# Performance work log

Measured on AMD Instinct MI355X. Metric: run time of the kernel, lower is better.

## Reference

```python
import jax, jax.numpy as jnp
import numpy as np

EMBED_DIM = 1024
NUM_HEADS = 16
HEAD_DIM = EMBED_DIM // NUM_HEADS


def setup_inputs() -> dict:
    key = jax.random.key(0)
    ks = jax.random.split(key, 5)
    B, S, D = 2, 2048, EMBED_DIM
    bound_qkv = 1.0 / np.sqrt(D)
    bound_out = 1.0 / np.sqrt(D)
    return {
        "x": jax.random.normal(ks[0], (B, S, D), dtype=jnp.float32),
        "w_qkv": jax.random.uniform(ks[1], (3 * D, D), jnp.float32, -bound_qkv, bound_qkv),
        "b_qkv": jax.random.uniform(ks[2], (3 * D,), jnp.float32, -bound_qkv, bound_qkv),
        "w_out": jax.random.uniform(ks[3], (D, D), jnp.float32, -bound_out, bound_out),
        "b_out": jax.random.uniform(ks[4], (D,), jnp.float32, -bound_out, bound_out),
    }


def reference(x, w_qkv, b_qkv, w_out, b_out):
    B, S, D = x.shape
    H, Hd = NUM_HEADS, HEAD_DIM
    qkv = x @ w_qkv.T + b_qkv                      # [B,S,3D]
    q, k, v = jnp.split(qkv, 3, axis=-1)           # each [B,S,D]
    # [B,S,D] -> [B,H,S,Hd]
    q = q.reshape(B, S, H, Hd).transpose(0, 2, 1, 3)
    k = k.reshape(B, S, H, Hd).transpose(0, 2, 1, 3)
    v = v.reshape(B, S, H, Hd).transpose(0, 2, 1, 3)
    scores = jnp.einsum("bhqd,bhkd->bhqk", q, k) / np.sqrt(Hd).astype(np.float32)
    probs = jax.nn.softmax(scores, axis=-1)
    attn = jnp.einsum("bhqk,bhkd->bhqd", probs, v)  # [B,H,S,Hd]
    attn = attn.transpose(0, 2, 1, 3).reshape(B, S, D)
    return attn @ w_out.T + b_out
```

## Files before the change

### kernel.cpp

```cpp
#include <hip/hip_runtime.h>

typedef __bf16 bf16_t;
typedef bf16_t bf16x4 __attribute__((ext_vector_type(4)));
typedef bf16_t bf16x8 __attribute__((ext_vector_type(8)));
typedef float f32x4 __attribute__((ext_vector_type(4)));
typedef float f32x16 __attribute__((ext_vector_type(16)));
typedef unsigned short u16;

#define MFMA16(a, b, c) __builtin_amdgcn_mfma_f32_16x16x32_bf16((a), (b), (c), 0, 0, 0)
#define MFMA32(a, b, c) __builtin_amdgcn_mfma_f32_32x32x16_bf16((a), (b), (c), 0, 0, 0)

#define BATCH 2
#define SEQ   2048
#define DIM   1024
#define NH    16
#define HD    64
#define ROWS  (BATCH * SEQ)
#define QKVN  (3 * DIM)
#define GK    1024

__device__ __forceinline__ u16 f2bf(float f) {
    unsigned u = __float_as_uint(f);
    u += 0x7FFFu + ((u >> 16) & 1u);
    return (u16)(u >> 16);
}

__device__ __forceinline__ float exp2_fast(float x) {
    float r;
    asm("v_exp_f32 %0, %1" : "=v"(r) : "v"(x));
    return r;
}

#define PKBF(lo_, hi_) ({ unsigned r_; \
    asm("v_cvt_pk_bf16_f32 %0, %1, %2" : "=v"(r_) : "v"(lo_), "v"(hi_)); r_; })
#define PLSWAP(a_, b_) \
    asm volatile("v_permlane32_swap_b32 %0, %1" : "+v"(a_), "+v"(b_))

#define GLDS(src, dst) __builtin_amdgcn_global_load_lds( \
    (const __attribute__((address_space(1))) void*)(src), \
    (__attribute__((address_space(3))) void*)(dst), 16, 0, 0)

#define WAITB(n) do { \
    asm volatile("s_waitcnt vmcnt(" #n ")" ::: "memory"); \
    __builtin_amdgcn_s_barrier(); } while (0)

__global__ __launch_bounds__(256) void cvt_kernel(
    const float* __restrict__ x,  u16* __restrict__ xb,  int nx4,
    const float* __restrict__ w1, u16* __restrict__ w1b, int n14,
    const float* __restrict__ w2, u16* __restrict__ w2b, int n24)
{
    const int total = nx4 + n14 + n24;
    for (int i = blockIdx.x * 256 + threadIdx.x; i < total; i += gridDim.x * 256) {
        const float4* s; ushort4* d; int o;
        if (i < nx4)             { s = (const float4*)x;  d = (ushort4*)xb;  o = i; }
        else if (i < nx4 + n14)  { s = (const float4*)w1; d = (ushort4*)w1b; o = i - nx4; }
        else                     { s = (const float4*)w2; d = (ushort4*)w2b; o = i - nx4 - n14; }
        float4 v = s[o];
        ushort4 r;
        r.x = f2bf(v.x); r.y = f2bf(v.y); r.z = f2bf(v.z); r.w = f2bf(v.w);
        d[o] = r;
    }
}

__global__ __launch_bounds__(512, 2) void gemm_qkv256(
    const u16* __restrict__ A, const u16* __restrict__ Bt,
    const float* __restrict__ bias, u16* __restrict__ C)
{
    __shared__ u16 As[2][256 * 64];
    __shared__ u16 Bs[2][256 * 64];

    const int tid  = threadIdx.x;
    const int lane = tid & 63;
    const int wave = tid >> 6;
    const int r16  = lane & 15;
    const int grp  = lane >> 4;
    const int wm   = wave >> 2, wn = wave & 3;

    int v = (int)blockIdx.x;
    v = (v & 7) * 24 + (v >> 3);
    const int tm = v / 12, tn = v - tm * 12;
    const size_t brow = (size_t)tm * 256;
    const size_t bcol = (size_t)tn * 256;

    const int srow = tid >> 3;
    const int aoff = ((tid & 7) ^ (srow & 7)) * 8;
    const u16* pA = A  + (brow + srow) * (size_t)GK + aoff;
    const u16* pB = Bt + (bcol + srow) * (size_t)GK + aoff;

    f32x4 acc[8][4];
    const f32x4 fz = {0.f, 0.f, 0.f, 0.f};
    #pragma unroll
    for (int m = 0; m < 8; ++m)
        #pragma unroll
        for (int n = 0; n < 4; ++n) acc[m][n] = fz;

    const int sw = r16 & 7;
    #define LDA256(buf, mh, mm, ks) \
        (*(const bf16x8*)&(buf)[(wm*128 + (mh)*64 + (mm)*16 + r16)*64 + ((((ks)*4+grp)^sw)*8)])
    #define LDB256(buf, n, ks) \
        (*(const bf16x8*)&(buf)[(wn*64 + (n)*16 + r16)*64 + ((((ks)*4+grp)^sw)*8)])

    {
        u16* Ad = &As[0][(wave * 8) * 64];
        u16* Bd = &Bs[0][(wave * 8) * 64];
        GLDS(pA, Ad);                 GLDS(pA + 64 * GK,  Ad + 64 * 64);
        GLDS(pA + 128 * GK, Ad + 128 * 64); GLDS(pA + 192 * GK, Ad + 192 * 64);
        GLDS(pB, Bd);                 GLDS(pB + 64 * GK,  Bd + 64 * 64);
        GLDS(pB + 128 * GK, Bd + 128 * 64); GLDS(pB + 192 * GK, Bd + 192 * 64);
    }

    for (int kt = 0; kt < GK / 64; ++kt) {
        const int cur  = kt & 1;
        const bool last = (kt == GK / 64 - 1);
        const int nk = (kt + 1) * 64;
        const u16* Ab = &As[cur][0];
        const u16* Bb = &Bs[cur][0];
        u16* Ad = &As[cur ^ 1][(wave * 8) * 64];
        u16* Bd = &Bs[cur ^ 1][(wave * 8) * 64];
        bf16x8 a[4][2], b0[2][2], b1[2][2];

        if (!last) {
            GLDS(pA + nk, Ad); GLDS(pA + 64 * GK + nk, Ad + 64 * 64);
            asm volatile("s_waitcnt vmcnt(2)" ::: "memory");
        } else {
            asm volatile("s_waitcnt vmcnt(0)" ::: "memory");
        }
        __builtin_amdgcn_s_barrier();
        #pragma unroll
        for (int mm = 0; mm < 4; ++mm) {
            a[mm][0] = LDA256(Ab, 0, mm, 0); a[mm][1] = LDA256(Ab, 0, mm, 1);
        }
        #pragma unroll
        for (int nn = 0; nn < 2; ++nn) {
            b0[nn][0] = LDB256(Bb, nn, 0); b0[nn][1] = LDB256(Bb, nn, 1);
        }
        __builtin_amdgcn_s_setprio(1);
        #pragma unroll
        for (int mm = 0; mm < 4; ++mm)
            #pragma unroll
            for (int nn = 0; nn < 2; ++nn) {
                acc[mm][nn] = MFMA16(a[mm][0], b0[nn][0], acc[mm][nn]);
                acc[mm][nn] = MFMA16(a[mm][1], b0[nn][1], acc[mm][nn]);
            }
        __builtin_amdgcn_s_setprio(0);
        __builtin_amdgcn_s_barrier();

        if (!last) { GLDS(pA + 128 * GK + nk, Ad + 128 * 64);
                     GLDS(pA + 192 * GK + nk, Ad + 192 * 64); }
        #pragma unroll
        for (int nn = 0; nn < 2; ++nn) {
            b1[nn][0] = LDB256(Bb, nn + 2, 0); b1[nn][1] = LDB256(Bb, nn + 2, 1);
        }
        __builtin_amdgcn_s_setprio(1);
        #pragma unroll
        for (int mm = 0; mm < 4; ++mm)
            #pragma unroll
            for (int nn = 0; nn < 2; ++nn) {
                acc[mm][nn + 2] = MFMA16(a[mm][0], b1[nn][0], acc[mm][nn + 2]);
                acc[mm][nn + 2] = MFMA16(a[mm][1], b1[nn][1], acc[mm][nn + 2]);
            }
        __builtin_amdgcn_s_setprio(0);
        __builtin_amdgcn_s_barrier();

        if (!last) { GLDS(pB + nk, Bd); GLDS(pB + 64 * GK + nk, Bd + 64 * 64); }
        #pragma unroll
        for (int mm = 0; mm < 4; ++mm) {
            a[mm][0] = LDA256(Ab, 1, mm, 0); a[mm][1] = LDA256(Ab, 1, mm, 1);
        }
        __builtin_amdgcn_s_setprio(1);
        #pragma unroll
        for (int mm = 0; mm < 4; ++mm)
            #pragma unroll
            for (int nn = 0; nn < 2; ++nn) {
                acc[mm + 4][nn + 2] = MFMA16(a[mm][0], b1[nn][0], acc[mm + 4][nn + 2]);
                acc[mm + 4][nn + 2] = MFMA16(a[mm][1], b1[nn][1], acc[mm + 4][nn + 2]);
            }
        __builtin_amdgcn_s_setprio(0);
        __builtin_amdgcn_s_barrier();

        if (!last) { GLDS(pB + 128 * GK + nk, Bd + 128 * 64);
                     GLDS(pB + 192 * GK + nk, Bd + 192 * 64); }
        __builtin_amdgcn_s_setprio(1);
        #pragma unroll
        for (int mm = 0; mm < 4; ++mm)
            #pragma unroll
            for (int nn = 0; nn < 2; ++nn) {
                acc[mm + 4][nn] = MFMA16(a[mm][0], b0[nn][0], acc[mm + 4][nn]);
                acc[mm + 4][nn] = MFMA16(a[mm][1], b0[nn][1], acc[mm + 4][nn]);
            }
        __builtin_amdgcn_s_setprio(0);
        __builtin_amdgcn_s_barrier();
    }

    #pragma unroll
    for (int n = 0; n < 4; ++n) {
        const size_t col = bcol + wn * 64 + n * 16 + r16;
        const float bv = bias[col];
        #pragma unroll
        for (int m = 0; m < 8; ++m) {
            const size_t row0 = brow + wm * 128 + m * 16 + grp * 4;
            if (tn >= 8) {
                const int c2 = (int)col - 2 * DIM;
                const int d = c2 & 63, h = c2 >> 6;
                const int bb = (int)(row0 >> 11), s0 = (int)(row0 & 2047);
                ushort4 pv;
                pv.x = f2bf(acc[m][n][0] + bv);
                pv.y = f2bf(acc[m][n][1] + bv);
                pv.z = f2bf(acc[m][n][2] + bv);
                pv.w = f2bf(acc[m][n][3] + bv);
                u16* dst = C + ((size_t)bb * 2048 + d * 32 + (s0 >> 6)) * (size_t)QKVN
                             + 2 * DIM + h * 64 + (s0 & 63);
                *(ushort4*)dst = pv;
            } else {
                #pragma unroll
                for (int i = 0; i < 4; ++i)
                    C[(row0 + i) * (size_t)QKVN + col] = f2bf(acc[m][n][i] + bv);
            }
        }
    }
    #undef LDA256
    #undef LDB256
}

__global__ __launch_bounds__(256) void gemm_bt(
    const u16* __restrict__ A, const u16* __restrict__ Bt,
    const float* __restrict__ bias, float* __restrict__ Cv,
    int M, int N, int K)
{
    __shared__ u16 As[128 * 64];
    __shared__ u16 Bs[64 * 64];

    const int tid  = threadIdx.x;
    const int lane = tid & 63;
    const int wave = tid >> 6;
    const int r16  = lane & 15;
    const int grp  = lane >> 4;

    const int nt  = N >> 6;
    const int nwg = (M >> 7) * nt;
    int v = blockIdx.x;
    if ((nwg & 7) == 0) { const int cpx = nwg >> 3; v = (v & 7) * cpx + (v >> 3); }
    const int tm = v / nt, tn = v - tm * nt;
    const size_t brow = (size_t)tm << 7;
    const size_t bcol = (size_t)tn << 6;

    const int wr = wave >> 1, wc = wave & 1;

    f32x4 acc[4][2];
    const f32x4 fz = {0.f, 0.f, 0.f, 0.f};
    #pragma unroll
    for (int m = 0; m < 4; ++m)
        #pragma unroll
        for (int n = 0; n < 2; ++n) acc[m][n] = fz;

    for (int kt = 0; kt < K; kt += 64) {
        #pragma unroll
        for (int it = 0; it < 4; ++it) {
            const int c = it * 256 + tid;
            const u16* ga = A + (brow + (c >> 3)) * (size_t)K + kt + (c & 7) * 8;
            GLDS(ga, &As[(it * 256 + wave * 64) * 8]);
        }
        #pragma unroll
        for (int it = 0; it < 2; ++it) {
            const int c = it * 256 + tid;
            const u16* gb = Bt + (bcol + (c >> 3)) * (size_t)K + kt + (c & 7) * 8;
            GLDS(gb, &Bs[(it * 256 + wave * 64) * 8]);
        }
        __syncthreads();
        #pragma unroll
        for (int ks = 0; ks < 2; ++ks) {
            bf16x8 af[4], bfr[2];
            #pragma unroll
            for (int m = 0; m < 4; ++m)
                af[m] = *(const bf16x8*)&As[(wr * 64 + m * 16 + r16) * 64 + ks * 32 + grp * 8];
            #pragma unroll
            for (int n = 0; n < 2; ++n)
                bfr[n] = *(const bf16x8*)&Bs[(wc * 32 + n * 16 + r16) * 64 + ks * 32 + grp * 8];
            #pragma unroll
            for (int m = 0; m < 4; ++m)
                #pragma unroll
                for (int n = 0; n < 2; ++n)
                    acc[m][n] = MFMA16(af[m], bfr[n], acc[m][n]);
        }
        __syncthreads();
    }

    #pragma unroll
    for (int n = 0; n < 2; ++n) {
        const size_t col = bcol + wc * 32 + n * 16 + r16;
        const float bv = bias[col];
        #pragma unroll
        for (int m = 0; m < 4; ++m) {
            const size_t row0 = brow + wr * 64 + m * 16 + grp * 4;
            #pragma unroll
            for (int i = 0; i < 4; ++i)
                Cv[(row0 + i) * (size_t)N + col] = acc[m][n][i] + bv;
        }
    }
}

__global__ __launch_bounds__(256, 2) void attn_kernel(
    const u16* __restrict__ qkv, u16* __restrict__ attb)
{
    __shared__ u16 kbuf[4][64 * 64];
    __shared__ u16 vbuf[4][64 * 64];

    const int tid  = threadIdx.x;
    const int lane = tid & 63;
    const int wave = tid >> 6;
    const int l31  = lane & 31;
    const int hi   = lane >> 5;
    const int k7   = l31 & 7;

    int v = (int)blockIdx.x;
    v = (v & 7) * 64 + (v >> 3);
    const int bh = v >> 4, qblk = v & 15;
    const int b  = bh >> 4, h = bh & 15;
    const int bS = b * SEQ;
    const int q0w = qblk * 128 + wave * 32;

    bf16x8 qf[4];
    {
        const u16* qp = qkv + (size_t)(bS + q0w + l31) * QKVN + h * HD + hi * 8;
        #pragma unroll
        for (int m = 0; m < 4; ++m) qf[m] = *(const bf16x8*)(qp + m * 16);
    }

    const f32x16 fz16 = {0,0,0,0,0,0,0,0,0,0,0,0,0,0,0,0};
    f32x16 o0 = fz16, o1 = fz16;
    float lsum = 0.f;

    const int r0 = wave * 16 + (lane >> 3);
    const int r1 = r0 + 8;
    const u16* kbase = qkv + (size_t)bS * QKVN + DIM + h * HD;
    const char* kp0 = (const char*)(kbase + (size_t)r0 * QKVN)
                      + (((lane & 7) * 16) ^ ((r0 & 7) << 4));
    const char* kp1 = (const char*)(kbase + (size_t)r1 * QKVN)
                      + (((lane & 7) * 16) ^ ((r1 & 7) << 4));
    const u16* vtb = qkv + (size_t)bS * QKVN + 2 * DIM + h * HD;
    const char* vp0 = (const char*)(vtb + (size_t)(r0 * 32) * QKVN)
                      + (((lane & 7) * 16) ^ ((r0 & 7) << 4));
    const char* vp1 = (const char*)(vtb + (size_t)(r1 * 32) * QKVN)
                      + (((lane & 7) * 16) ^ ((r1 & 7) << 4));

    auto stage = [&](int bsel) {
        u16* kd = &kbuf[bsel][(wave * 16) * 64];
        u16* vd = &vbuf[bsel][(wave * 16) * 64];
        GLDS(kp0, kd);
        GLDS(kp1, kd + 8 * 64);
        GLDS(vp0, vd);
        GLDS(vp1, vd + 8 * 64);
        kp0 += 64 * QKVN * 2; kp1 += 64 * QKVN * 2;
        vp0 += QKVN * 2;      vp1 += QKVN * 2;
    };

    const float C1 = 0.125f * 1.44269504f;
    const float C2 = -8.0f * 1.44269504f;

    auto compute_tile = [&](const u16* kb_, const u16* vb_) {
        const char* kc = (const char*)kb_;
        const char* vc = (const char*)vb_;
        bf16x8 paf[4];

        #pragma unroll
        for (int kt = 0; kt < 2; ++kt) {
            bf16x8 kf[4];
            #pragma unroll
            for (int m = 0; m < 4; ++m)
                kf[m] = *(const bf16x8*)(kc + (kt * 32 + l31) * 128
                                            + (((m * 2 + hi) ^ k7) * 16));
            f32x16 s = fz16;
            __builtin_amdgcn_s_setprio(1);
            #pragma unroll
            for (int m = 0; m < 4; ++m) s = MFMA32(kf[m], qf[m], s);
            __builtin_amdgcn_s_setprio(0);

            float p[16];
            #pragma unroll
            for (int r = 0; r < 16; ++r) {
                p[r] = exp2_fast(fmaf(s[r], C1, C2));
                lsum += p[r];
            }
            unsigned A = PKBF(p[0], p[1]),  Bw = PKBF(p[2], p[3]);
            unsigned C = PKBF(p[4], p[5]),  D  = PKBF(p[6], p[7]);
            unsigned E = PKBF(p[8], p[9]),  F  = PKBF(p[10], p[11]);
            unsigned G = PKBF(p[12], p[13]), H = PKBF(p[14], p[15]);
            PLSWAP(A, C); PLSWAP(Bw, D); PLSWAP(E, G); PLSWAP(F, H);
            union { unsigned u[4]; bf16x8 v8; } w0 = {{A, Bw, C, D}},
                                                w1 = {{E, F, G, H}};
            paf[kt * 2]     = w0.v8;
            paf[kt * 2 + 1] = w1.v8;
        }

        __builtin_amdgcn_s_setprio(1);
        #pragma unroll
        for (int m2 = 0; m2 < 4; ++m2) {
            const int cs = ((m2 * 2 + hi) ^ k7) * 16;
            const bf16x8 vf0 = *(const bf16x8*)(vc + l31 * 128 + cs);
            const bf16x8 vf1 = *(const bf16x8*)(vc + (32 + l31) * 128 + cs);
            o0 = MFMA32(paf[m2], vf0, o0);
            o1 = MFMA32(paf[m2], vf1, o1);
        }
        __builtin_amdgcn_s_setprio(0);
    };

    stage(0); stage(1); stage(2);

    for (int i = 0; i < 7; ++i) {
        WAITB(8); stage(3); compute_tile(&kbuf[0][0], &vbuf[0][0]);
        WAITB(8); stage(0); compute_tile(&kbuf[1][0], &vbuf[1][0]);
        WAITB(8); stage(1); compute_tile(&kbuf[2][0], &vbuf[2][0]);
        WAITB(8); stage(2); compute_tile(&kbuf[3][0], &vbuf[3][0]);
    }
    WAITB(8); stage(3); compute_tile(&kbuf[0][0], &vbuf[0][0]);
    WAITB(8);           compute_tile(&kbuf[1][0], &vbuf[1][0]);
    WAITB(4);           compute_tile(&kbuf[2][0], &vbuf[2][0]);
    WAITB(0);           compute_tile(&kbuf[3][0], &vbuf[3][0]);

    const float ltot = lsum + __shfl_xor(lsum, 32, 64);
    const float rinv = 1.0f / ltot;

    u16* ob = attb + (size_t)(bS + q0w) * DIM + h * HD + l31;
    #pragma unroll
    for (int r = 0; r < 16; ++r) {
        const int q = (r & 3) + 8 * (r >> 2) + 4 * hi;
        const float iv = __shfl(rinv, q, 64);
        u16* pr = ob + (size_t)q * DIM;
        pr[0]  = f2bf(o0[r] * iv);
        pr[32] = f2bf(o1[r] * iv);
    }
}

extern "C" void kernel_launch(void* const* d_in, const int* in_sizes, int n_in,
                              void* d_out, int out_size, void* d_ws, size_t ws_size,
                              hipStream_t stream)
{
    const float* x     = (const float*)d_in[0];
    const float* w_qkv = (const float*)d_in[1];
    const float* b_qkv = (const float*)d_in[2];
    const float* w_out = (const float*)d_in[3];
    const float* b_out = (const float*)d_in[4];
    float* out = (float*)d_out;

    u16* ws   = (u16*)d_ws;
    u16* XB   = ws;
    u16* WQB  = ws + 4194304;
    u16* WOB  = ws + 7340032;
    u16* QKVB = ws + 8388608;
    u16* ATTB = ws + 20971520;

    cvt_kernel<<<2048, 256, 0, stream>>>(x, XB, (ROWS * DIM) / 4,
                                         w_qkv, WQB, (QKVN * DIM) / 4,
                                         w_out, WOB, (DIM * DIM) / 4);

    gemm_qkv256<<<(ROWS / 256) * (QKVN / 256), 512, 0, stream>>>(
        XB, WQB, b_qkv, QKVB);

    attn_kernel<<<BATCH * NH * (SEQ / 128), 256, 0, stream>>>(QKVB, ATTB);

    gemm_bt<<<(ROWS / 128) * (DIM / 64), 256, 0, stream>>>(
        ATTB, WOB, b_out, out, ROWS, DIM, GK);
}
```

Baseline: 123.0 us.

## Split attention KV sequence across two wave groups with LDS reduction

The attention block grows from 256 to 512 threads. Each half of the waves processes half of the key/value sequence with its own double-buffered LDS staging, replacing the previous four-deep pipeline. After the loop, the second half writes its partial outputs and row sums to LDS and the first half adds them before normalising and storing. This doubles the waves per block to hide latency, at the cost of a shallower prefetch, full vmcnt waits each tile, and an extra LDS reduction step.

```diff
diff --git a/kernel.cpp b/kernel.cpp
--- a/kernel.cpp
+++ b/kernel.cpp
@@ -299,15 +299,17 @@
     }
 }
 
-__global__ __launch_bounds__(256, 2) void attn_kernel(
+__global__ __launch_bounds__(512, 4) void attn_kernel(
     const u16* __restrict__ qkv, u16* __restrict__ attb)
 {
-    __shared__ u16 kbuf[4][64 * 64];
-    __shared__ u16 vbuf[4][64 * 64];
+    __shared__ u16 smem[8][64 * 64];
 
     const int tid  = threadIdx.x;
     const int lane = tid & 63;
     const int wave = tid >> 6;
+    const int half = wave >> 2;
+    const int w4   = wave & 3;
+    const int hb   = half * 4;
     const int l31  = lane & 31;
     const int hi   = lane >> 5;
     const int k7   = l31 & 7;
@@ -317,7 +319,7 @@
     const int bh = v >> 4, qblk = v & 15;
     const int b  = bh >> 4, h = bh & 15;
     const int bS = b * SEQ;
-    const int q0w = qblk * 128 + wave * 32;
+    const int q0w = qblk * 128 + w4 * 32;
 
     bf16x8 qf[4];
     {
@@ -330,22 +332,22 @@
     f32x16 o0 = fz16, o1 = fz16;
     float lsum = 0.f;
 
-    const int r0 = wave * 16 + (lane >> 3);
+    const int r0 = w4 * 16 + (lane >> 3);
     const int r1 = r0 + 8;
     const u16* kbase = qkv + (size_t)bS * QKVN + DIM + h * HD;
-    const char* kp0 = (const char*)(kbase + (size_t)r0 * QKVN)
+    const char* kp0 = (const char*)(kbase + (size_t)(r0 + half * 1024) * QKVN)
                       + (((lane & 7) * 16) ^ ((r0 & 7) << 4));
-    const char* kp1 = (const char*)(kbase + (size_t)r1 * QKVN)
+    const char* kp1 = (const char*)(kbase + (size_t)(r1 + half * 1024) * QKVN)
                       + (((lane & 7) * 16) ^ ((r1 & 7) << 4));
     const u16* vtb = qkv + (size_t)bS * QKVN + 2 * DIM + h * HD;
-    const char* vp0 = (const char*)(vtb + (size_t)(r0 * 32) * QKVN)
+    const char* vp0 = (const char*)(vtb + (size_t)(r0 * 32 + half * 16) * QKVN)
                       + (((lane & 7) * 16) ^ ((r0 & 7) << 4));
-    const char* vp1 = (const char*)(vtb + (size_t)(r1 * 32) * QKVN)
+    const char* vp1 = (const char*)(vtb + (size_t)(r1 * 32 + half * 16) * QKVN)
                       + (((lane & 7) * 16) ^ ((r1 & 7) << 4));
 
     auto stage = [&](int bsel) {
-        u16* kd = &kbuf[bsel][(wave * 16) * 64];
-        u16* vd = &vbuf[bsel][(wave * 16) * 64];
+        u16* kd = &smem[hb + bsel][(w4 * 16) * 64];
+        u16* vd = &smem[hb + 2 + bsel][(w4 * 16) * 64];
         GLDS(kp0, kd);
         GLDS(kp1, kd + 8 * 64);
         GLDS(vp0, vd);
@@ -404,30 +406,50 @@
         __builtin_amdgcn_s_setprio(0);
     };
 
-    stage(0); stage(1); stage(2);
-
-    for (int i = 0; i < 7; ++i) {
-        WAITB(8); stage(3); compute_tile(&kbuf[0][0], &vbuf[0][0]);
-        WAITB(8); stage(0); compute_tile(&kbuf[1][0], &vbuf[1][0]);
-        WAITB(8); stage(1); compute_tile(&kbuf[2][0], &vbuf[2][0]);
-        WAITB(8); stage(2); compute_tile(&kbuf[3][0], &vbuf[3][0]);
-    }
-    WAITB(8); stage(3); compute_tile(&kbuf[0][0], &vbuf[0][0]);
-    WAITB(8);           compute_tile(&kbuf[1][0], &vbuf[1][0]);
-    WAITB(4);           compute_tile(&kbuf[2][0], &vbuf[2][0]);
-    WAITB(0);           compute_tile(&kbuf[3][0], &vbuf[3][0]);
-
-    const float ltot = lsum + __shfl_xor(lsum, 32, 64);
-    const float rinv = 1.0f / ltot;
-
-    u16* ob = attb + (size_t)(bS + q0w) * DIM + h * HD + l31;
-    #pragma unroll
-    for (int r = 0; r < 16; ++r) {
-        const int q = (r & 3) + 8 * (r >> 2) + 4 * hi;
-        const float iv = __shfl(rinv, q, 64);
-        u16* pr = ob + (size_t)q * DIM;
-        pr[0]  = f2bf(o0[r] * iv);
-        pr[32] = f2bf(o1[r] * iv);
+    stage(0);
+    asm volatile("s_waitcnt vmcnt(0)" ::: "memory");
+    __builtin_amdgcn_s_barrier();
+
+    for (int it = 0; it < 8; ++it) {
+        stage(1);
+        compute_tile(&smem[hb][0], &smem[hb + 2][0]);
+        WAITB(0);
+        if (it < 7) stage(0);
+        compute_tile(&smem[hb + 1][0], &smem[hb + 3][0]);
+        WAITB(0);
+    }
+
+    float* obuf = (float*)&smem[0][0];
+    const int cidx = (w4 * 64 + lane) * 36;
+    if (half == 1) {
+        #pragma unroll
+        for (int r = 0; r < 16; ++r) {
+            obuf[cidx + r]      = o0[r];
+            obuf[cidx + 16 + r] = o1[r];
+        }
+        obuf[cidx + 32] = lsum;
+    }
+    __syncthreads();
+    if (half == 0) {
+        #pragma unroll
+        for (int r = 0; r < 16; ++r) {
+            o0[r] += obuf[cidx + r];
+            o1[r] += obuf[cidx + 16 + r];
+        }
+        lsum += obuf[cidx + 32];
+
+        const float ltot = lsum + __shfl_xor(lsum, 32, 64);
+        const float rinv = 1.0f / ltot;
+
+        u16* ob = attb + (size_t)(bS + q0w) * DIM + h * HD + l31;
+        #pragma unroll
+        for (int r = 0; r < 16; ++r) {
+            const int q = (r & 3) + 8 * (r >> 2) + 4 * hi;
+            const float iv = __shfl(rinv, q, 64);
+            u16* pr = ob + (size_t)q * DIM;
+            pr[0]  = f2bf(o0[r] * iv);
+            pr[32] = f2bf(o1[r] * iv);
+        }
     }
 }
 
@@ -456,7 +478,7 @@
     gemm_qkv256<<<(ROWS / 256) * (QKVN / 256), 512, 0, stream>>>(
         XB, WQB, b_qkv, QKVB);
 
-    attn_kernel<<<BATCH * NH * (SEQ / 128), 256, 0, stream>>>(QKVB, ATTB);
+    attn_kernel<<<BATCH * NH * (SEQ / 128), 512, 0, stream>>>(QKVB, ATTB);
 
     gemm_bt<<<(ROWS / 128) * (DIM / 64), 256, 0, stream>>>(
         ATTB, WOB, b_out, out, ROWS, DIM, GK);
```

New measurement: 121.3 us. No clear change (-1.4%).
